# Kernel tuning notes

Hardware: AMD Instinct MI355X
Metric: run time of the kernel (lower is better)

## Reference

```python
import jax, jax.numpy as jnp
import numpy as np


def setup_inputs() -> dict:
    key = jax.random.key(0)
    k1, k2 = jax.random.split(key)
    B, D, H, W = 16, 256, 32, 32
    K = 2048
    z = jax.random.normal(k1, (B, D, H, W), dtype=jnp.float32)
    # EmbeddingEMA init: uniform(-1/K, 1/K); plain randn scaled works as a stand-in param
    codebook = jax.random.uniform(k2, (K, D), dtype=jnp.float32,
                                  minval=-1.0 / K, maxval=1.0 / K)
    return {"z": z, "codebook": codebook}


def reference(z, codebook):
    # z: (B, D, H, W) -> (B, H, W, D) -> (n, D)   [normalize == 'none' path]
    B, D, H, W = z.shape
    z_flat = jnp.transpose(z, (0, 2, 3, 1)).reshape(-1, D)          # (n, D)
    z_norm = z_flat
    codebook_norm = codebook                                         # (K, D)

    # squared L2 distance: ||z||^2 + ||c||^2 - 2 z c^T   -> (n, K)
    distance = (jnp.sum(z_norm * z_norm, axis=1, keepdims=True)
                + jnp.sum(codebook_norm * codebook_norm, axis=1)
                - 2.0 * jnp.matmul(z_norm, codebook_norm.T))

    vq_indices = jnp.argmin(distance, axis=1)                        # (n,)
    z_q = codebook_norm[vq_indices]                                  # gather (n, D)

    # straight-through estimator (standard VQ forward output)
    z_q_st = z_norm + jax.lax.stop_gradient(z_q - z_norm)
    out = z_q_st.reshape(B, H, W, D).transpose(0, 3, 1, 2)           # (B, D, H, W)
    return out
```

## Files before the change

### kernel.cpp

```cpp
#include <hip/hip_runtime.h>
#include <stdint.h>


#define D_    256
#define K_    2048
#define HW_   1024
#define MT    64
#define NT    256
#define KT    16
#define SPLIT 2
#define KS    (K_ / SPLIT)
#define CST   260
#define BUFSZ (KT * MT + KT * CST)
#define NPIX  16384

__device__ __forceinline__ void gload16(const float* g, float* l) {
    auto* gp = reinterpret_cast<const __attribute__((address_space(1))) uint32_t*>(
        reinterpret_cast<uintptr_t>(g));
    auto* lp = reinterpret_cast<__attribute__((address_space(3))) uint32_t*>(
        reinterpret_cast<uintptr_t>(l));
    __builtin_amdgcn_global_load_lds(gp, lp, 16, 0, 0);
}

__device__ __forceinline__ float pw8(const float r[8]) {
    float t01 = __fadd_rn(r[0], r[1]);
    float t23 = __fadd_rn(r[2], r[3]);
    float L   = __fadd_rn(t01, t23);
    float t45 = __fadd_rn(r[4], r[5]);
    float t67 = __fadd_rn(r[6], r[7]);
    float R   = __fadd_rn(t45, t67);
    return __fadd_rn(L, R);
}

__global__ __launch_bounds__(256) void prep_k(const float* __restrict__ z,
                                              const float* __restrict__ cb,
                                              float* __restrict__ ct,
                                              float* __restrict__ An,
                                              float* __restrict__ Bn) {
    __shared__ float t[64][65];
    int tid = threadIdx.x;
    int bx  = blockIdx.x;
    if (bx < 128) {
        int k0 = (bx & 31) << 6;
        int d0 = (bx >> 5) << 6;
        #pragma unroll
        for (int it = 0; it < 4; ++it) {
            int u  = (it << 8) + tid;
            int kk = u >> 4;
            int dd = (u & 15) << 2;
            float4 v = *reinterpret_cast<const float4*>(
                cb + (size_t)(k0 + kk) * D_ + d0 + dd);
            t[kk][dd + 0] = v.x; t[kk][dd + 1] = v.y;
            t[kk][dd + 2] = v.z; t[kk][dd + 3] = v.w;
        }
        __syncthreads();
        #pragma unroll
        for (int it = 0; it < 4; ++it) {
            int u  = (it << 8) + tid;
            int dd = u >> 4;
            int kk = (u & 15) << 2;
            float4 o;
            o.x = t[kk + 0][dd]; o.y = t[kk + 1][dd];
            o.z = t[kk + 2][dd]; o.w = t[kk + 3][dd];
            *reinterpret_cast<float4*>(ct + (size_t)(d0 + dd) * K_ + k0 + kk) = o;
        }
    } else if (bx < 136) {
        int row = (bx - 128) * 256 + tid;
        const float4* p = reinterpret_cast<const float4*>(cb + (size_t)row * D_);
        float rA[8], rB[8];
        #pragma unroll
        for (int j = 0; j < 8; ++j) { rA[j] = 0.f; rB[j] = 0.f; }
        #pragma unroll
        for (int q = 0; q < 64; ++q) {
            float4 v = p[q];
            float pv[4] = {__fmul_rn(v.x, v.x), __fmul_rn(v.y, v.y),
                           __fmul_rn(v.z, v.z), __fmul_rn(v.w, v.w)};
            if (q < 32) {
                #pragma unroll
                for (int l = 0; l < 4; ++l)
                    rA[(4 * q + l) & 7] = __fadd_rn(rA[(4 * q + l) & 7], pv[l]);
            } else {
                #pragma unroll
                for (int l = 0; l < 4; ++l)
                    rB[(4 * q + l) & 7] = __fadd_rn(rB[(4 * q + l) & 7], pv[l]);
            }
        }
        Bn[row] = __fadd_rn(pw8(rA), pw8(rB));
    } else {
        int blk = bx - 136;
        int b   = blk >> 2;
        int hw0 = (blk & 3) << 8;
        const float* zb = z + (size_t)b * (D_ * HW_) + hw0 + tid;
        float rA[8], rB[8];
        #pragma unroll
        for (int j = 0; j < 8; ++j) { rA[j] = 0.f; rB[j] = 0.f; }
        #pragma unroll 8
        for (int d = 0; d < 128; ++d) {
            float v = zb[(size_t)d * HW_];
            rA[d & 7] = __fadd_rn(rA[d & 7], __fmul_rn(v, v));
        }
        #pragma unroll 8
        for (int d = 128; d < 256; ++d) {
            float v = zb[(size_t)d * HW_];
            rB[d & 7] = __fadd_rn(rB[d & 7], __fmul_rn(v, v));
        }
        An[(size_t)b * HW_ + hw0 + tid] = __fadd_rn(pw8(rA), pw8(rB));
    }
}

__global__ __launch_bounds__(256, 2) void vq_k(const float* __restrict__ z,
                                               const float* __restrict__ ct,
                                               const float* __restrict__ An,
                                               const float* __restrict__ Bn,
                                               float* __restrict__ pscore,
                                               int* __restrict__ pidx) {
    __shared__ float smem[2 * BUFSZ];
    float* rs = smem;
    int*   ri = (int*)(smem + MT * 33);

    const int tid  = threadIdx.x;
    const int lane = tid & 63;
    const int w    = tid >> 6;
    const int tn   = (tid & 7) | (w << 3);
    const int tm   = (tid >> 3) & 7;
    const int blk  = blockIdx.x;
    const int p    = blk >> 1;
    const int s    = blk & 1;
    const int b      = p >> 4;
    const int hwbase = (p & 15) << 6;
    const float* zbase = z + (size_t)b * (D_ * HW_) + hwbase;
    const float* ctS   = ct + s * KS;

    const float* zsrc = zbase + (size_t)((w << 2) + (lane >> 4)) * HW_
                              + ((lane & 15) << 2);

    float bs[8]; int bi[8];
    #pragma unroll
    for (int i = 0; i < 8; ++i) { bs[i] = 1e30f; bi[i] = 0; }
    float acc[8][8];
    #pragma unroll
    for (int i = 0; i < 8; ++i)
        #pragma unroll
        for (int j = 0; j < 8; ++j) acc[i][j] = 0.f;

    #define STAGE(ph)                                                         \
        do {                                                                  \
            int buf_ = (ph) & 1, kc_ = (ph) & 15, nc_ = (ph) >> 4;            \
            float* zb_ = smem + buf_ * BUFSZ;                                 \
            float* cb_ = zb_ + KT * MT;                                       \
            gload16(zsrc + (size_t)kc_ * (KT * HW_), zb_ + (w << 2) * MT);    \
            _Pragma("unroll")                                                 \
            for (int r = 0; r < 4; ++r) {                                     \
                int row = (w << 2) + r;                                       \
                gload16(ctS + (size_t)((kc_ << 4) + row) * K_ + nc_ * NT      \
                            + (lane << 2),                                    \
                        cb_ + row * CST);                                     \
            }                                                                 \
        } while (0)

    STAGE(0);

    for (int ph = 0; ph < 64; ++ph) {
        __syncthreads();
        if (ph < 63) STAGE(ph + 1);
        const float* zb_ = smem + (ph & 1) * BUFSZ;
        const float* cb_ = zb_ + KT * MT;
        #pragma unroll
        for (int d = 0; d < KT; ++d) {
            const float* zr = zb_ + d * MT + (tm << 3);
            float4 a0 = *reinterpret_cast<const float4*>(zr);
            float4 a1 = *reinterpret_cast<const float4*>(zr + 4);
            const float* cr = cb_ + d * CST + (tn << 3);
            float4 b0 = *reinterpret_cast<const float4*>(cr);
            float4 b1 = *reinterpret_cast<const float4*>(cr + 4);
            float av[8] = {a0.x, a0.y, a0.z, a0.w, a1.x, a1.y, a1.z, a1.w};
            float bv[8] = {b0.x, b0.y, b0.z, b0.w, b1.x, b1.y, b1.z, b1.w};
            #pragma unroll
            for (int i = 0; i < 8; ++i)
                #pragma unroll
                for (int j = 0; j < 8; ++j)
                    acc[i][j] = fmaf(av[i], bv[j], acc[i][j]);
        }
        if ((ph & 15) == 15) {
            int nc = ph >> 4;
            #pragma unroll
            for (int j = 0; j < 8; ++j) {
                int ng = s * KS + nc * NT + (tn << 3) + j;
                float bn = Bn[ng];
                #pragma unroll
                for (int i = 0; i < 8; ++i) {
                    float an = An[(size_t)b * HW_ + hwbase + (tm << 3) + i];
                    float sc = __fsub_rn(__fadd_rn(an, bn),
                                         __fmul_rn(2.0f, acc[i][j]));
                    if (sc < bs[i]) { bs[i] = sc; bi[i] = ng; }
                }
            }
            #pragma unroll
            for (int i = 0; i < 8; ++i)
                #pragma unroll
                for (int j = 0; j < 8; ++j) acc[i][j] = 0.f;
        }
    }
    #undef STAGE

    __syncthreads();
    #pragma unroll
    for (int i = 0; i < 8; ++i) {
        int m = (tm << 3) + i;
        rs[m * 33 + tn] = bs[i];
        ri[m * 33 + tn] = bi[i];
    }
    __syncthreads();
    if (tid < MT) {
        int   m    = tid;
        float best = rs[m * 33];
        int   bidx = ri[m * 33];
        for (int t = 1; t < 32; ++t) {
            float sv = rs[m * 33 + t];
            int   ix = ri[m * 33 + t];
            if (sv < best || (sv == best && ix < bidx)) { best = sv; bidx = ix; }
        }
        int g = b * HW_ + hwbase + m;
        pscore[s * NPIX + g] = best;
        pidx[s * NPIX + g]   = bidx;
    }
}

__global__ __launch_bounds__(256) void fin_k(const float* __restrict__ cb,
                                             const float* __restrict__ pscore,
                                             const int* __restrict__ pidx,
                                             float* __restrict__ out) {
    __shared__ int idxs[MT];
    int tid = threadIdx.x;
    int p   = blockIdx.x;
    int b      = p >> 4;
    int hwbase = (p & 15) << 6;
    if (tid < MT) {
        int g = b * HW_ + hwbase + tid;
        float best = pscore[g];
        int   bidx = pidx[g];
        #pragma unroll
        for (int s = 1; s < SPLIT; ++s) {
            float sv = pscore[s * NPIX + g];
            int   ix = pidx[s * NPIX + g];
            if (sv < best || (sv == best && ix < bidx)) { best = sv; bidx = ix; }
        }
        idxs[tid] = bidx;
    }
    __syncthreads();
    float* obase = out + (size_t)b * (D_ * HW_) + hwbase;
    #pragma unroll
    for (int it = 0; it < 16; ++it) {
        int u  = (it << 8) + tid;
        int dd = u >> 4;
        int m4 = u & 15;
        int i0 = idxs[(m4 << 2) + 0];
        int i1 = idxs[(m4 << 2) + 1];
        int i2 = idxs[(m4 << 2) + 2];
        int i3 = idxs[(m4 << 2) + 3];
        float4 o;
        o.x = cb[(size_t)i0 * D_ + dd];
        o.y = cb[(size_t)i1 * D_ + dd];
        o.z = cb[(size_t)i2 * D_ + dd];
        o.w = cb[(size_t)i3 * D_ + dd];
        *reinterpret_cast<float4*>(obase + (size_t)dd * HW_ + (m4 << 2)) = o;
    }
}

extern "C" void kernel_launch(void* const* d_in, const int* in_sizes, int n_in,
                              void* d_out, int out_size, void* d_ws, size_t ws_size,
                              hipStream_t stream) {
    const float* z  = (const float*)d_in[0];
    const float* cb = (const float*)d_in[1];
    float* pscore = (float*)d_ws;
    int*   pidx   = (int*)(pscore + SPLIT * NPIX);
    float* An     = (float*)(pidx + SPLIT * NPIX);
    float* Bn     = An + NPIX;
    float* ct     = Bn + K_;
    float* out    = (float*)d_out;

    prep_k<<<dim3(200), dim3(256), 0, stream>>>(z, cb, ct, An, Bn);
    vq_k<<<dim3(256 * SPLIT), dim3(256), 0, stream>>>(z, ct, An, Bn, pscore, pidx);
    fin_k<<<dim3(256), dim3(256), 0, stream>>>(cb, pscore, pidx, out);
}
```

Baseline: 294.0 us.

## Fuse argmin reduction and gather into VQ kernel with atomic last-block finalize

Pixel tiles grow from 64 to 128 (16x8 register accumulators per thread) and the codebook is split into 4 parts instead of 2. Partial argmin results are merged through 64-bit atomicMin on packed (score, index) keys, and the last block per tile, detected with an atomic counter, does the codebook gather and output write. This removes the separate finalize kernel launch and the partial-result round trip, and each loaded codebook slice is reused across more pixels. In exchange occupancy drops to one block per SIMD slot, register pressure rises, and correctness now depends on score bits ordering like unsigned integers, which holds only for non-negative scores.

```diff
diff --git a/kernel.cpp b/kernel.cpp
--- a/kernel.cpp
+++ b/kernel.cpp
@@ -5,13 +5,14 @@
 #define D_    256
 #define K_    2048
 #define HW_   1024
-#define MT    64
+#define MT    128
 #define NT    256
 #define KT    16
-#define SPLIT 2
+#define SPLIT 4
 #define KS    (K_ / SPLIT)
 #define CST   260
-#define BUFSZ (KT * MT + KT * CST)
+#define ZSZ   (KT * MT)
+#define BUFSZ (ZSZ + KT * CST)
 #define NPIX  16384
 
 __device__ __forceinline__ void gload16(const float* g, float* l) {
@@ -36,11 +37,14 @@
                                               const float* __restrict__ cb,
                                               float* __restrict__ ct,
                                               float* __restrict__ An,
-                                              float* __restrict__ Bn) {
+                                              float* __restrict__ Bn,
+                                              unsigned long long* __restrict__ keys,
+                                              int* __restrict__ cnt) {
     __shared__ float t[64][65];
     int tid = threadIdx.x;
     int bx  = blockIdx.x;
     if (bx < 128) {
+        if (bx == 0 && tid < MT) cnt[tid] = 0;
         int k0 = (bx & 31) << 6;
         int d0 = (bx >> 5) << 6;
         #pragma unroll
@@ -90,6 +94,7 @@
         int blk = bx - 136;
         int b   = blk >> 2;
         int hw0 = (blk & 3) << 8;
+        keys[(size_t)b * HW_ + hw0 + tid] = 0xFFFFFFFFFFFFFFFFull;
         const float* zb = z + (size_t)b * (D_ * HW_) + hw0 + tid;
         float rA[8], rB[8];
         #pragma unroll
@@ -108,15 +113,19 @@
     }
 }
 
-__global__ __launch_bounds__(256, 2) void vq_k(const float* __restrict__ z,
+__global__ __launch_bounds__(256, 1) void vq_k(const float* __restrict__ z,
                                                const float* __restrict__ ct,
+                                               const float* __restrict__ cb,
                                                const float* __restrict__ An,
                                                const float* __restrict__ Bn,
-                                               float* __restrict__ pscore,
-                                               int* __restrict__ pidx) {
+                                               unsigned long long* __restrict__ keys,
+                                               int* __restrict__ cnt,
+                                               float* __restrict__ out) {
     __shared__ float smem[2 * BUFSZ];
+    __shared__ int sflag;
     float* rs = smem;
     int*   ri = (int*)(smem + MT * 33);
+    int*   idxs = ri;
 
     const int tid  = threadIdx.x;
     const int lane = tid & 63;
@@ -124,22 +133,22 @@
     const int tn   = (tid & 7) | (w << 3);
     const int tm   = (tid >> 3) & 7;
     const int blk  = blockIdx.x;
-    const int p    = blk >> 1;
-    const int s    = blk & 1;
-    const int b      = p >> 4;
-    const int hwbase = (p & 15) << 6;
+    const int p    = blk >> 2;
+    const int s    = blk & 3;
+    const int b      = p >> 3;
+    const int hwbase = (p & 7) << 7;
     const float* zbase = z + (size_t)b * (D_ * HW_) + hwbase;
     const float* ctS   = ct + s * KS;
 
-    const float* zsrc = zbase + (size_t)((w << 2) + (lane >> 4)) * HW_
-                              + ((lane & 15) << 2);
-
-    float bs[8]; int bi[8];
+    const float* zsrc = zbase + (size_t)(lane >> 5) * HW_ + ((lane & 31) << 2);
+    const float* csrc = ctS + ((size_t)lane << 2);
+
+    float bs[16]; int bi[16];
     #pragma unroll
-    for (int i = 0; i < 8; ++i) { bs[i] = 1e30f; bi[i] = 0; }
-    float acc[8][8];
+    for (int i = 0; i < 16; ++i) { bs[i] = 1e30f; bi[i] = 0; }
+    float acc[16][8];
     #pragma unroll
-    for (int i = 0; i < 8; ++i)
+    for (int i = 0; i < 16; ++i)
         #pragma unroll
         for (int j = 0; j < 8; ++j) acc[i][j] = 0.f;
 
@@ -147,56 +156,68 @@
         do {                                                                  \
             int buf_ = (ph) & 1, kc_ = (ph) & 15, nc_ = (ph) >> 4;            \
             float* zb_ = smem + buf_ * BUFSZ;                                 \
-            float* cb_ = zb_ + KT * MT;                                       \
-            gload16(zsrc + (size_t)kc_ * (KT * HW_), zb_ + (w << 2) * MT);    \
+            float* cb_ = zb_ + ZSZ;                                           \
+            _Pragma("unroll")                                                 \
+            for (int t = 0; t < 2; ++t) {                                     \
+                int row = (w << 2) + (t << 1);                                \
+                gload16(zsrc + (size_t)(kc_ * KT + row) * HW_,                \
+                        zb_ + row * MT);                                      \
+            }                                                                 \
             _Pragma("unroll")                                                 \
             for (int r = 0; r < 4; ++r) {                                     \
                 int row = (w << 2) + r;                                       \
-                gload16(ctS + (size_t)((kc_ << 4) + row) * K_ + nc_ * NT      \
-                            + (lane << 2),                                    \
+                gload16(csrc + (size_t)(kc_ * KT + row) * K_ + nc_ * NT,      \
                         cb_ + row * CST);                                     \
             }                                                                 \
         } while (0)
 
     STAGE(0);
 
-    for (int ph = 0; ph < 64; ++ph) {
+    for (int ph = 0; ph < 32; ++ph) {
         __syncthreads();
-        if (ph < 63) STAGE(ph + 1);
+        if (ph < 31) STAGE(ph + 1);
         const float* zb_ = smem + (ph & 1) * BUFSZ;
-        const float* cb_ = zb_ + KT * MT;
+        const float* cb_ = zb_ + ZSZ;
         #pragma unroll
         for (int d = 0; d < KT; ++d) {
             const float* zr = zb_ + d * MT + (tm << 3);
             float4 a0 = *reinterpret_cast<const float4*>(zr);
             float4 a1 = *reinterpret_cast<const float4*>(zr + 4);
+            float4 a2 = *reinterpret_cast<const float4*>(zr + 64);
+            float4 a3 = *reinterpret_cast<const float4*>(zr + 68);
             const float* cr = cb_ + d * CST + (tn << 3);
             float4 b0 = *reinterpret_cast<const float4*>(cr);
             float4 b1 = *reinterpret_cast<const float4*>(cr + 4);
-            float av[8] = {a0.x, a0.y, a0.z, a0.w, a1.x, a1.y, a1.z, a1.w};
-            float bv[8] = {b0.x, b0.y, b0.z, b0.w, b1.x, b1.y, b1.z, b1.w};
-            #pragma unroll
-            for (int i = 0; i < 8; ++i)
+            float av[16] = {a0.x, a0.y, a0.z, a0.w, a1.x, a1.y, a1.z, a1.w,
+                            a2.x, a2.y, a2.z, a2.w, a3.x, a3.y, a3.z, a3.w};
+            float bv[8]  = {b0.x, b0.y, b0.z, b0.w, b1.x, b1.y, b1.z, b1.w};
+            #pragma unroll
+            for (int i = 0; i < 16; ++i)
                 #pragma unroll
                 for (int j = 0; j < 8; ++j)
                     acc[i][j] = fmaf(av[i], bv[j], acc[i][j]);
         }
         if ((ph & 15) == 15) {
             int nc = ph >> 4;
+            float an[16];
+            #pragma unroll
+            for (int i = 0; i < 16; ++i) {
+                int m = (i < 8) ? ((tm << 3) + i) : (64 + (tm << 3) + i - 8);
+                an[i] = An[(size_t)b * HW_ + hwbase + m];
+            }
             #pragma unroll
             for (int j = 0; j < 8; ++j) {
                 int ng = s * KS + nc * NT + (tn << 3) + j;
                 float bn = Bn[ng];
                 #pragma unroll
-                for (int i = 0; i < 8; ++i) {
-                    float an = An[(size_t)b * HW_ + hwbase + (tm << 3) + i];
-                    float sc = __fsub_rn(__fadd_rn(an, bn),
+                for (int i = 0; i < 16; ++i) {
+                    float sc = __fsub_rn(__fadd_rn(an[i], bn),
                                          __fmul_rn(2.0f, acc[i][j]));
                     if (sc < bs[i]) { bs[i] = sc; bi[i] = ng; }
                 }
             }
             #pragma unroll
-            for (int i = 0; i < 8; ++i)
+            for (int i = 0; i < 16; ++i)
                 #pragma unroll
                 for (int j = 0; j < 8; ++j) acc[i][j] = 0.f;
         }
@@ -205,65 +226,52 @@
 
     __syncthreads();
     #pragma unroll
-    for (int i = 0; i < 8; ++i) {
-        int m = (tm << 3) + i;
+    for (int i = 0; i < 16; ++i) {
+        int m = (i < 8) ? ((tm << 3) + i) : (64 + (tm << 3) + i - 8);
         rs[m * 33 + tn] = bs[i];
         ri[m * 33 + tn] = bi[i];
     }
     __syncthreads();
+    unsigned long long* keyp = keys + (size_t)b * HW_ + hwbase;
     if (tid < MT) {
-        int   m    = tid;
-        float best = rs[m * 33];
-        int   bidx = ri[m * 33];
+        float best = rs[tid * 33];
+        int   bidx = ri[tid * 33];
         for (int t = 1; t < 32; ++t) {
-            float sv = rs[m * 33 + t];
-            int   ix = ri[m * 33 + t];
+            float sv = rs[tid * 33 + t];
+            int   ix = ri[tid * 33 + t];
             if (sv < best || (sv == best && ix < bidx)) { best = sv; bidx = ix; }
         }
-        int g = b * HW_ + hwbase + m;
-        pscore[s * NPIX + g] = best;
-        pidx[s * NPIX + g]   = bidx;
-    }
-}
-
-__global__ __launch_bounds__(256) void fin_k(const float* __restrict__ cb,
-                                             const float* __restrict__ pscore,
-                                             const int* __restrict__ pidx,
-                                             float* __restrict__ out) {
-    __shared__ int idxs[MT];
-    int tid = threadIdx.x;
-    int p   = blockIdx.x;
-    int b      = p >> 4;
-    int hwbase = (p & 15) << 6;
-    if (tid < MT) {
-        int g = b * HW_ + hwbase + tid;
-        float best = pscore[g];
-        int   bidx = pidx[g];
-        #pragma unroll
-        for (int s = 1; s < SPLIT; ++s) {
-            float sv = pscore[s * NPIX + g];
-            int   ix = pidx[s * NPIX + g];
-            if (sv < best || (sv == best && ix < bidx)) { best = sv; bidx = ix; }
-        }
-        idxs[tid] = bidx;
-    }
-    __syncthreads();
-    float* obase = out + (size_t)b * (D_ * HW_) + hwbase;
-    #pragma unroll
-    for (int it = 0; it < 16; ++it) {
-        int u  = (it << 8) + tid;
-        int dd = u >> 4;
-        int m4 = u & 15;
-        int i0 = idxs[(m4 << 2) + 0];
-        int i1 = idxs[(m4 << 2) + 1];
-        int i2 = idxs[(m4 << 2) + 2];
-        int i3 = idxs[(m4 << 2) + 3];
-        float4 o;
-        o.x = cb[(size_t)i0 * D_ + dd];
-        o.y = cb[(size_t)i1 * D_ + dd];
-        o.z = cb[(size_t)i2 * D_ + dd];
-        o.w = cb[(size_t)i3 * D_ + dd];
-        *reinterpret_cast<float4*>(obase + (size_t)dd * HW_ + (m4 << 2)) = o;
+        unsigned long long key =
+            ((unsigned long long)__float_as_uint(best) << 32) | (unsigned)bidx;
+        atomicMin(keyp + tid, key);
+    }
+    __threadfence();
+    __syncthreads();
+    if (tid == 0) sflag = atomicAdd(cnt + p, 1);
+    __syncthreads();
+    if (sflag == 3) {
+        if (tid < MT) {
+            unsigned long long v = atomicMin(keyp + tid, 0xFFFFFFFFFFFFFFFFull);
+            idxs[tid] = (int)(unsigned)v;
+        }
+        __syncthreads();
+        float* obase = out + (size_t)b * (D_ * HW_) + hwbase;
+        #pragma unroll
+        for (int it = 0; it < 32; ++it) {
+            int u  = (it << 8) + tid;
+            int dd = u >> 5;
+            int c4 = u & 31;
+            int i0 = idxs[(c4 << 2) + 0];
+            int i1 = idxs[(c4 << 2) + 1];
+            int i2 = idxs[(c4 << 2) + 2];
+            int i3 = idxs[(c4 << 2) + 3];
+            float4 o;
+            o.x = cb[(size_t)i0 * D_ + dd];
+            o.y = cb[(size_t)i1 * D_ + dd];
+            o.z = cb[(size_t)i2 * D_ + dd];
+            o.w = cb[(size_t)i3 * D_ + dd];
+            *reinterpret_cast<float4*>(obase + (size_t)dd * HW_ + (c4 << 2)) = o;
+        }
     }
 }
 
@@ -272,14 +280,14 @@
                               hipStream_t stream) {
     const float* z  = (const float*)d_in[0];
     const float* cb = (const float*)d_in[1];
-    float* pscore = (float*)d_ws;
-    int*   pidx   = (int*)(pscore + SPLIT * NPIX);
-    float* An     = (float*)(pidx + SPLIT * NPIX);
-    float* Bn     = An + NPIX;
-    float* ct     = Bn + K_;
-    float* out    = (float*)d_out;
-
-    prep_k<<<dim3(200), dim3(256), 0, stream>>>(z, cb, ct, An, Bn);
-    vq_k<<<dim3(256 * SPLIT), dim3(256), 0, stream>>>(z, ct, An, Bn, pscore, pidx);
-    fin_k<<<dim3(256), dim3(256), 0, stream>>>(cb, pscore, pidx, out);
-}
+    unsigned long long* keys = (unsigned long long*)d_ws;
+    int*   cnt = (int*)(keys + NPIX);
+    float* An  = (float*)(cnt + MT);
+    float* Bn  = An + NPIX;
+    float* ct  = Bn + K_;
+    float* out = (float*)d_out;
+
+    prep_k<<<dim3(200), dim3(256), 0, stream>>>(z, cb, ct, An, Bn, keys, cnt);
+    vq_k<<<dim3(128 * SPLIT), dim3(256), 0, stream>>>(z, ct, cb, An, Bn,
+                                                      keys, cnt, out);
+}
```

After: 392.9 us. 33.7% more time.
